# Performance work log

Hardware: AMD Instinct MI355X
Metric: run time of the kernel (lower is better)

Reference implementation:

```python
import jax, jax.numpy as jnp
import numpy as np

# dims: NL layers, D=d_model, DI=expand*D, F=d_ff, V=vocab, L=S*C seq, R=dt_rank, N=d_state, K=d_conv
NL, D, DI, F, V, L, R, N, K = 2, 256, 512, 1024, 1024, 1024, 16, 16, 4
B, S, C = 2, 128, 8
EPS = 1e-5


def silu(x):
    return x * jax.nn.sigmoid(x)


def batchnorm(x, g, b):  # x: [B,L,D], normalize over (B,L) per channel (training-mode BatchNorm1d)
    m = x.mean((0, 1))
    v = x.var((0, 1))
    return (x - m) * jax.lax.rsqrt(v + EPS) * g + b


def layernorm(x, g, b):
    m = x.mean(-1, keepdims=True)
    v = x.var(-1, keepdims=True)
    return (x - m) * jax.lax.rsqrt(v + EPS) * g + b


def mamba(x, Win, cw, cb, Wx, Wdt, bdt, A_log, Dsk, Wout, bout):
    # x: [B,L,D] -> [B,L,D]; standard Mamba block with selective scan
    Bsz, Lseq, _ = x.shape
    xz = x @ Win                      # [B,L,2*DI]
    xi, z = jnp.split(xz, 2, axis=-1)
    # depthwise causal conv1d, width K
    xp = jnp.pad(xi, ((0, 0), (K - 1, 0), (0, 0)))
    xc = cb + sum(xp[:, k:k + Lseq, :] * cw[:, k] for k in range(K))
    xc = silu(xc)                     # [B,L,DI]
    xdb = xc @ Wx                     # [B,L,R+2N]
    delta = jax.nn.softplus(xdb[..., :R] @ Wdt + bdt)   # [B,L,DI]
    Bm = xdb[..., R:R + N]            # [B,L,N]
    Cm = xdb[..., R + N:]             # [B,L,N]
    A = -jnp.exp(A_log)               # [DI,N]
    dA = jnp.exp(delta[..., None] * A)                       # [B,L,DI,N]
    dBx = delta[..., None] * Bm[:, :, None, :] * xc[..., None]  # [B,L,DI,N]

    def step(h, inp):
        dA_t, dBx_t, C_t = inp
        h = h * dA_t + dBx_t          # [B,DI,N]
        y = jnp.einsum('bdn,bn->bd', h, C_t)
        return h, y

    h0 = jnp.zeros((Bsz, DI, N), x.dtype)
    _, ys = jax.lax.scan(step, h0, (dA.transpose(1, 0, 2, 3), dBx.transpose(1, 0, 2, 3), Cm.transpose(1, 0, 2)))
    y = ys.transpose(1, 0, 2) + Dsk * xc
    y = y * silu(z)
    return y @ Wout + bout


def _forward(input_ids, emb, pos, Win, conv_w, conv_b, Wx, Wdt, bdt, A_log, Dskip, Wout, bout,
             bn_g, bn_b, ln_g, ln_b, ff_w1, ff_b1, ff_w2, ff_b2, final_w, final_b):
    Bsz, Ssz, Csz = input_ids.shape
    Lseq = Ssz * Csz
    # Encoder: token embedding (scaled) + learned positions, flattened to [B, S*C, D]
    x = emb[input_ids].reshape(Bsz, Lseq, D) * jnp.sqrt(jnp.float32(D)) + pos[:Lseq]
    for i in range(NL):
        f = mamba(x, Win[i, 0], conv_w[i, 0], conv_b[i, 0], Wx[i, 0], Wdt[i, 0], bdt[i, 0],
                  A_log[i, 0], Dskip[i, 0], Wout[i, 0], bout[i, 0])
        f = batchnorm(f, bn_g[i, 0], bn_b[i, 0])
        bk = mamba(x[:, ::-1], Win[i, 1], conv_w[i, 1], conv_b[i, 1], Wx[i, 1], Wdt[i, 1], bdt[i, 1],
                   A_log[i, 1], Dskip[i, 1], Wout[i, 1], bout[i, 1])
        bk = batchnorm(bk, bn_g[i, 1], bn_b[i, 1])[:, ::-1]
        f = layernorm(x + f, ln_g[i, 0], ln_b[i, 0])
        bk = layernorm(x + bk, ln_g[i, 1], ln_b[i, 1])
        out = f + bk
        out = jax.nn.relu(out @ ff_w1[i] + ff_b1[i]) @ ff_w2[i] + ff_b2[i]
        out = batchnorm(out, bn_g[i, 2], bn_b[i, 2])
        x = out + x
    return x.reshape(Bsz, Ssz, Csz, D) @ final_w + final_b   # [B,S,C,V]


def setup_inputs() -> dict:
    key = jax.random.key(0)
    ks = list(jax.random.split(key, 16))
    kit = iter(ks)
    rn = lambda shape, s=0.02: jax.random.normal(next(kit), shape, jnp.float32) * s
    inp = {
        'input_ids': jax.random.randint(next(kit), (B, S, C), 0, V),
        'emb': rn((V, D)), 'pos': rn((L, D)),
        'Win': rn((NL, 2, D, 2 * DI)),
        'conv_w': rn((NL, 2, DI, K), 0.1), 'conv_b': jnp.zeros((NL, 2, DI)),
        'Wx': rn((NL, 2, DI, R + 2 * N)),
        'Wdt': rn((NL, 2, R, DI)), 'bdt': jnp.full((NL, 2, DI), -4.0),
        'A_log': jnp.broadcast_to(jnp.log(jnp.arange(1, N + 1, dtype=jnp.float32)), (NL, 2, DI, N)) + 0.0,
        'Dskip': jnp.ones((NL, 2, DI)),
        'Wout': rn((NL, 2, DI, D)), 'bout': jnp.zeros((NL, 2, D)),
        'bn_g': jnp.ones((NL, 3, D)), 'bn_b': jnp.zeros((NL, 3, D)),
        'ln_g': jnp.ones((NL, 2, D)), 'ln_b': jnp.zeros((NL, 2, D)),
        'ff_w1': rn((NL, D, F)), 'ff_b1': jnp.zeros((NL, F)),
        'ff_w2': rn((NL, F, D)), 'ff_b2': jnp.zeros((NL, D)),
        'final_w': rn((D, V)), 'final_b': jnp.zeros((V,)),
    }
    return inp


def reference(input_ids, emb, pos, Win, conv_w, conv_b, Wx, Wdt, bdt, A_log, Dskip, Wout, bout,
              bn_g, bn_b, ln_g, ln_b, ff_w1, ff_b1, ff_w2, ff_b2, final_w, final_b):
    return _forward(input_ids, emb, pos, Win, conv_w, conv_b, Wx, Wdt, bdt, A_log, Dskip, Wout, bout,
                    bn_g, bn_b, ln_g, ln_b, ff_w1, ff_b1, ff_w2, ff_b2, final_w, final_b)
```

## Files before the change

kernel.cpp:

```cpp
#include <hip/hip_runtime.h>

#define NL 2
#define DMODEL 256
#define DI 512
#define FF 1024
#define VV 1024
#define LSEQ 1024
#define RR 16
#define NN 16
#define KCONV 4
#define BTOK 2048
#define EPS 1e-5f

using short8 = __attribute__((ext_vector_type(8))) short;
using float4v = __attribute__((ext_vector_type(4))) float;
typedef unsigned short u16;

__device__ inline float bf2f(u16 u) {
    union { unsigned u; float f; } x; x.u = (unsigned)u << 16; return x.f;
}
__device__ inline u16 f2bf(float f) {
    union { float f; unsigned u; } x; x.f = f;
    unsigned r = x.u + 0x7fffu + ((x.u >> 16) & 1u);
    return (u16)(r >> 16);
}

#if __has_builtin(__builtin_amdgcn_exp2f)
#define EXP2(x) __builtin_amdgcn_exp2f(x)
#else
#define EXP2(x) exp2f(x)
#endif

struct TMat { const float* src; u16* dst; int rows, cols, tile0, tilecols; };
struct TTable { TMat m[24]; int nmat; };

__global__ __launch_bounds__(256) void transpose_kernel(TTable tt) {
    __shared__ u16 tile[32][33];
    int bx = blockIdx.x;
    int j = 0;
    for (int k = 1; k < tt.nmat; ++k) if (bx >= tt.m[k].tile0) j = k;
    TMat mm = tt.m[j];
    int lt = bx - mm.tile0;
    int r0 = (lt / mm.tilecols) * 32, c0 = (lt % mm.tilecols) * 32;
    int tx = threadIdx.x & 31, ty = threadIdx.x >> 5;
    #pragma unroll
    for (int k = 0; k < 4; ++k) {
        int r = r0 + ty + k * 8, c = c0 + tx;
        tile[ty + k * 8][tx] = (r < mm.rows && c < mm.cols) ? f2bf(mm.src[(size_t)r * mm.cols + c]) : (u16)0;
    }
    __syncthreads();
    #pragma unroll
    for (int k = 0; k < 4; ++k) {
        int c = c0 + ty + k * 8, r = r0 + tx;
        if (c < mm.cols && r < mm.rows) mm.dst[(size_t)c * mm.rows + r] = tile[tx][ty + k * 8];
    }
}

__global__ __launch_bounds__(256) void gemm_kernel(
    const u16* __restrict__ A0, int lda, unsigned long long sA,
    const u16* __restrict__ B0, int ldb, unsigned long long sB,
    const float* __restrict__ bias0, unsigned long long sBias,
    void* __restrict__ C0, int ldc, unsigned long long sC,
    int M, int N, int K, int act, int outfp)
{
    const u16* A = A0 + (size_t)blockIdx.z * sA;
    const u16* Bt = B0 + (size_t)blockIdx.z * sB;
    const float* bias = bias0 ? (bias0 + (size_t)blockIdx.z * sBias) : nullptr;

    int tid = threadIdx.x;
    int wv = tid >> 6, lane = tid & 63;
    int row0 = blockIdx.y * 64 + (wv >> 1) * 32;
    int col0 = blockIdx.x * 64 + (wv & 1) * 32;
    int mi = lane & 15, kq = lane >> 4;

    float4v acc[2][2];
    #pragma unroll
    for (int a = 0; a < 2; ++a)
        #pragma unroll
        for (int b = 0; b < 2; ++b) acc[a][b] = (float4v){0.f, 0.f, 0.f, 0.f};
    const short8 zer = {0, 0, 0, 0, 0, 0, 0, 0};

    for (int kk = 0; kk < K; kk += 32) {
        int k = kk + kq * 8;
        bool kv = (k < K);
        short8 af[2], bf[2];
        #pragma unroll
        for (int rt = 0; rt < 2; ++rt) {
            int r = row0 + rt * 16 + mi;
            af[rt] = kv ? *(const short8*)(A + (size_t)r * lda + k) : zer;
        }
        #pragma unroll
        for (int ct = 0; ct < 2; ++ct) {
            int n = col0 + ct * 16 + mi;
            bf[ct] = (kv && n < N) ? *(const short8*)(Bt + (size_t)n * ldb + k) : zer;
        }
        #pragma unroll
        for (int rt = 0; rt < 2; ++rt)
            #pragma unroll
            for (int ct = 0; ct < 2; ++ct)
                acc[rt][ct] = __builtin_amdgcn_mfma_f32_16x16x32_bf16(af[rt], bf[ct], acc[rt][ct], 0, 0, 0);
    }

    #pragma unroll
    for (int rt = 0; rt < 2; ++rt)
        #pragma unroll
        for (int ct = 0; ct < 2; ++ct) {
            int n = col0 + ct * 16 + mi;
            if (n >= N) continue;
            float bv = bias ? bias[n] : 0.f;
            #pragma unroll
            for (int r = 0; r < 4; ++r) {
                int m = row0 + rt * 16 + kq * 4 + r;
                float v = acc[rt][ct][r] + bv;
                if (act == 1) v = fmaxf(v, 0.f);
                if (outfp)
                    ((float*)C0)[(size_t)blockIdx.z * sC + (size_t)m * ldc + n] = v;
                else
                    ((u16*)C0)[(size_t)blockIdx.z * sC + (size_t)m * ldc + n] = f2bf(v);
            }
        }
}

__global__ __launch_bounds__(256) void delta_fused_kernel(
    const u16* __restrict__ xdb, const u16* __restrict__ wdtT,
    const float* __restrict__ bdt, const u16* __restrict__ xc,
    u16* __restrict__ deltaT, u16* __restrict__ uT, int layer)
{
    int z = blockIdx.z;
    const u16* A = xdb + (size_t)z * BTOK * 48;
    const u16* Bt = wdtT + (size_t)z * 512 * 16;
    const float* bias = bdt + (size_t)z * 512;

    int tid = threadIdx.x;
    int wv = tid >> 6, lane = tid & 63;
    int row0 = blockIdx.y * 64 + (wv >> 1) * 32;
    int col0 = blockIdx.x * 64 + (wv & 1) * 32;
    int mi = lane & 15, kq = lane >> 4;

    float4v acc[2][2];
    #pragma unroll
    for (int a = 0; a < 2; ++a)
        #pragma unroll
        for (int b = 0; b < 2; ++b) acc[a][b] = (float4v){0.f, 0.f, 0.f, 0.f};
    const short8 zer = {0, 0, 0, 0, 0, 0, 0, 0};

    int k = kq * 8;
    bool kv = (k < 16);
    short8 af[2], bf[2];
    #pragma unroll
    for (int rt = 0; rt < 2; ++rt) {
        int r = row0 + rt * 16 + mi;
        af[rt] = kv ? *(const short8*)(A + (size_t)r * 48 + k) : zer;
    }
    #pragma unroll
    for (int ct = 0; ct < 2; ++ct) {
        int n = col0 + ct * 16 + mi;
        bf[ct] = kv ? *(const short8*)(Bt + (size_t)n * 16 + k) : zer;
    }
    #pragma unroll
    for (int rt = 0; rt < 2; ++rt)
        #pragma unroll
        for (int ct = 0; ct < 2; ++ct)
            acc[rt][ct] = __builtin_amdgcn_mfma_f32_16x16x32_bf16(af[rt], bf[ct], acc[rt][ct], 0, 0, 0);

    #pragma unroll
    for (int rt = 0; rt < 2; ++rt)
        #pragma unroll
        for (int ct = 0; ct < 2; ++ct) {
            int n = col0 + ct * 16 + mi;
            float bv = bias[n];
            #pragma unroll
            for (int r = 0; r < 4; ++r) {
                int m = row0 + rt * 16 + kq * 4 + r;
                float v = acc[rt][ct][r] + bv;
                v = (v > 20.f) ? v : logf(1.f + __expf(v));
                float xcv = bf2f(xc[((size_t)z * BTOK + m) * DI + n]);
                int b = m >> 10, t = m & 1023;
                size_t off = ((size_t)((z * 2 + b) * DI + n)) * LSEQ + t;
                deltaT[off] = f2bf(v);
                uT[off] = f2bf(v * xcv);
            }
        }
}

__global__ __launch_bounds__(256) void embed_kernel(
    const int* __restrict__ ids, const float* __restrict__ emb,
    const float* __restrict__ pos, u16* __restrict__ x)
{
    int tok = blockIdx.x, d = threadIdx.x;
    int id = ids[tok];
    float v = emb[(size_t)id * DMODEL + d] * 16.0f + pos[(size_t)(tok & (LSEQ - 1)) * DMODEL + d];
    x[(size_t)tok * DMODEL + d] = f2bf(v);
}

__global__ __launch_bounds__(256) void conv_kernel(
    const u16* __restrict__ xz, const float* __restrict__ conv_w,
    const float* __restrict__ conv_b, u16* __restrict__ xc, int layer)
{
    unsigned g = blockIdx.x * 256u + threadIdx.x;
    int d = g & 511;
    int t = (g >> 9) & 1023;
    int b = (g >> 19) & 1;
    int dir = g >> 20;
    int wbase = ((layer * 2 + dir) * DI + d);
    float acc = conv_b[wbase];
    int colbase = dir * 1024 + d;
    #pragma unroll
    for (int k = 0; k < KCONV; ++k) {
        int ts = dir ? (t + 3 - k) : (t - 3 + k);
        if (ts >= 0 && ts < LSEQ)
            acc += conv_w[wbase * KCONV + k] * bf2f(xz[(size_t)((b << 10) + ts) * 2048 + colbase]);
    }
    float v = acc / (1.f + __expf(-acc));
    xc[(size_t)(((dir * 2 + b) << 10) + t) * DI + d] = f2bf(v);
}

#define SCC 128
#define SCS 8
#define SLDS (2 * SCC * 17)

template<int DIR>
__device__ __forceinline__ void scan_body(
    const u16* __restrict__ deltaT, const u16* __restrict__ uT,
    const u16* __restrict__ xdb, const float* __restrict__ A_log,
    u16* __restrict__ pT, int layer, int slab,
    float* Ps, float* Qs)
{
    int tid = threadIdx.x;
    int c = tid & 127, dloc = tid >> 7;
    int d = blockIdx.x * 2 + dloc;

    float a2[16];
    const float* al = A_log + (size_t)(((layer * 2 + DIR) * DI + d) * NN);
    #pragma unroll
    for (int n = 0; n < 16; ++n) a2[n] = -__expf(al[n]) * 1.44269504f;

    const size_t tb = ((size_t)(slab * DI + d)) * LSEQ;
    const int rowb = slab << 10;
    const int T0 = DIR ? (1016 - 8 * c) : (8 * c);

    short8 dlv = *(const short8*)(deltaT + tb + T0);
    short8 uvv = *(const short8*)(uT + tb + T0);

    float P[16], Q[16];
    #pragma unroll
    for (int n = 0; n < 16; ++n) { P[n] = 1.f; Q[n] = 0.f; }
    #pragma unroll
    for (int j = 0; j < 8; ++j) {
        const int idx = DIR ? 7 - j : j;
        float dl = bf2f((u16)dlv[idx]);
        float uv = bf2f((u16)uvv[idx]);
        const u16* xr = xdb + (size_t)(rowb + T0 + idx) * 48;
        short8 b0 = *(const short8*)(xr + 16);
        short8 b1 = *(const short8*)(xr + 24);
        #pragma unroll
        for (int n = 0; n < 8; ++n) {
            float dA = EXP2(dl * a2[n]);
            Q[n] = Q[n] * dA + uv * bf2f((u16)b0[n]);
            P[n] *= dA;
        }
        #pragma unroll
        for (int n = 0; n < 8; ++n) {
            float dA = EXP2(dl * a2[8 + n]);
            Q[8 + n] = Q[8 + n] * dA + uv * bf2f((u16)b1[n]);
            P[8 + n] *= dA;
        }
    }
    int base = (dloc * 128 + c) * 17;
    #pragma unroll
    for (int n = 0; n < 16; ++n) { Ps[base + n] = P[n]; Qs[base + n] = Q[n]; }
    __syncthreads();

    if (tid < 32) {
        int n = tid & 15, dl2 = tid >> 4;
        float h = 0.f;
        for (int cc = 0; cc < 128; ++cc) {
            int o = (dl2 * 128 + cc) * 17 + n;
            float p_ = Ps[o], q_ = Qs[o];
            Ps[o] = h;
            h = p_ * h + q_;
        }
    }
    __syncthreads();

    float h[16];
    #pragma unroll
    for (int n = 0; n < 16; ++n) h[n] = Ps[base + n];
    short8 pk;
    #pragma unroll
    for (int j = 0; j < 8; ++j) {
        const int idx = DIR ? 7 - j : j;
        float dl = bf2f((u16)dlv[idx]);
        float uv = bf2f((u16)uvv[idx]);
        const u16* xr = xdb + (size_t)(rowb + T0 + idx) * 48;
        short8 b0 = *(const short8*)(xr + 16);
        short8 b1 = *(const short8*)(xr + 24);
        short8 c0 = *(const short8*)(xr + 32);
        short8 c1 = *(const short8*)(xr + 40);
        float pacc[4] = {0.f, 0.f, 0.f, 0.f};
        #pragma unroll
        for (int n = 0; n < 8; ++n) {
            float dA = EXP2(dl * a2[n]);
            h[n] = h[n] * dA + uv * bf2f((u16)b0[n]);
            pacc[n & 3] = fmaf(h[n], bf2f((u16)c0[n]), pacc[n & 3]);
        }
        #pragma unroll
        for (int n = 0; n < 8; ++n) {
            float dA = EXP2(dl * a2[8 + n]);
            h[8 + n] = h[8 + n] * dA + uv * bf2f((u16)b1[n]);
            pacc[n & 3] = fmaf(h[8 + n], bf2f((u16)c1[n]), pacc[n & 3]);
        }
        pk[idx] = (short)f2bf((pacc[0] + pacc[1]) + (pacc[2] + pacc[3]));
    }
    *(short8*)(pT + tb + T0) = pk;
}

__global__ __launch_bounds__(256) void scan_kernel(
    const u16* __restrict__ deltaT, const u16* __restrict__ uT,
    const u16* __restrict__ xdb, const float* __restrict__ A_log,
    u16* __restrict__ pT, int layer)
{
    __shared__ float Ps[SLDS], Qs[SLDS];
    int slab = blockIdx.y;
    if (slab >> 1)
        scan_body<1>(deltaT, uT, xdb, A_log, pT, layer, slab, Ps, Qs);
    else
        scan_body<0>(deltaT, uT, xdb, A_log, pT, layer, slab, Ps, Qs);
}

__global__ __launch_bounds__(256) void gate_kernel(
    const u16* __restrict__ pT, const u16* __restrict__ xc,
    const u16* __restrict__ xz, const float* __restrict__ Dskip,
    u16* __restrict__ y, int layer)
{
    __shared__ float tile[32][33];
    int z = blockIdx.z, dir = z >> 1, b = z & 1;
    int d0 = blockIdx.x * 32, t0 = blockIdx.y * 32;
    int tx = threadIdx.x & 31, ty = threadIdx.x >> 5;
    #pragma unroll
    for (int k = 0; k < 4; ++k) {
        int d = d0 + ty + k * 8;
        tile[ty + k * 8][tx] = bf2f(pT[((size_t)(z * DI + d)) * LSEQ + t0 + tx]);
    }
    __syncthreads();
    #pragma unroll
    for (int k = 0; k < 4; ++k) {
        int t = t0 + ty + k * 8, d = d0 + tx;
        float p = tile[tx][ty + k * 8];
        float xcv = bf2f(xc[(size_t)((z << 10) + t) * DI + d]);
        float zv = bf2f(xz[(size_t)((b << 10) + t) * 2048 + dir * 1024 + 512 + d]);
        float dsk = Dskip[(layer * 2 + dir) * DI + d];
        float yv = (p + dsk * xcv) * (zv / (1.f + __expf(-zv)));
        y[(size_t)((z << 10) + t) * DI + d] = f2bf(yv);
    }
}

__global__ __launch_bounds__(256) void bnstats_kernel(
    const u16* __restrict__ p0, const u16* __restrict__ p1, float* __restrict__ stats)
{
    int d = blockIdx.x, arr = blockIdx.y, tid = threadIdx.x;
    const u16* p = arr ? p1 : p0;
    float s = 0.f, q = 0.f;
    #pragma unroll
    for (int k = 0; k < 8; ++k) {
        float v = bf2f(p[(size_t)(tid + k * 256) * DMODEL + d]);
        s += v; q += v * v;
    }
    #pragma unroll
    for (int off = 1; off < 64; off <<= 1) { s += __shfl_xor(s, off); q += __shfl_xor(q, off); }
    __shared__ float ss[4], qs[4];
    if ((tid & 63) == 0) { ss[tid >> 6] = s; qs[tid >> 6] = q; }
    __syncthreads();
    if (tid == 0) {
        float S = ss[0] + ss[1] + ss[2] + ss[3];
        float Q2 = qs[0] + qs[1] + qs[2] + qs[3];
        float mean = S * (1.f / 2048.f);
        float var = Q2 * (1.f / 2048.f) - mean * mean;
        stats[(arr * DMODEL + d) * 2] = mean;
        stats[(arr * DMODEL + d) * 2 + 1] = rsqrtf(var + EPS);
    }
}

__global__ __launch_bounds__(256) void fuseln_kernel(
    const u16* __restrict__ x, const u16* __restrict__ outm, const float* __restrict__ stats,
    const float* __restrict__ bng, const float* __restrict__ bnb,
    const float* __restrict__ lng, const float* __restrict__ lnb, u16* __restrict__ ffin)
{
    int tok = blockIdx.x, d = threadIdx.x;
    float xv = bf2f(x[(size_t)tok * DMODEL + d]);
    float of = bf2f(outm[(size_t)tok * DMODEL + d]);
    float ob = bf2f(outm[(size_t)BTOK * DMODEL + (size_t)tok * DMODEL + d]);
    float vf = xv + (of - stats[d * 2]) * stats[d * 2 + 1] * bng[d] + bnb[d];
    float vb = xv + (ob - stats[(DMODEL + d) * 2]) * stats[(DMODEL + d) * 2 + 1] * bng[DMODEL + d] + bnb[DMODEL + d];
    float s0 = vf, s1 = vf * vf, s2 = vb, s3 = vb * vb;
    #pragma unroll
    for (int off = 1; off < 64; off <<= 1) {
        s0 += __shfl_xor(s0, off); s1 += __shfl_xor(s1, off);
        s2 += __shfl_xor(s2, off); s3 += __shfl_xor(s3, off);
    }
    __shared__ float sm[4][4];
    if ((d & 63) == 0) { sm[d >> 6][0] = s0; sm[d >> 6][1] = s1; sm[d >> 6][2] = s2; sm[d >> 6][3] = s3; }
    __syncthreads();
    s0 = sm[0][0] + sm[1][0] + sm[2][0] + sm[3][0];
    s1 = sm[0][1] + sm[1][1] + sm[2][1] + sm[3][1];
    s2 = sm[0][2] + sm[1][2] + sm[2][2] + sm[3][2];
    s3 = sm[0][3] + sm[1][3] + sm[2][3] + sm[3][3];
    float mf = s0 * (1.f / 256.f), vvf = s1 * (1.f / 256.f) - mf * mf;
    float mb = s2 * (1.f / 256.f), vvb = s3 * (1.f / 256.f) - mb * mb;
    float fl = (vf - mf) * rsqrtf(vvf + EPS) * lng[d] + lnb[d];
    float bl = (vb - mb) * rsqrtf(vvb + EPS) * lng[DMODEL + d] + lnb[DMODEL + d];
    ffin[(size_t)tok * DMODEL + d] = f2bf(fl + bl);
}

__global__ __launch_bounds__(256) void bnadd_kernel(
    u16* __restrict__ x, const u16* __restrict__ ffo, const float* __restrict__ stats,
    const float* __restrict__ g, const float* __restrict__ b)
{
    int tok = blockIdx.x, d = threadIdx.x;
    size_t idx = (size_t)tok * DMODEL + d;
    float v = bf2f(x[idx]) + (bf2f(ffo[idx]) - stats[d * 2]) * stats[d * 2 + 1] * g[d] + b[d];
    x[idx] = f2bf(v);
}

extern "C" void kernel_launch(void* const* d_in, const int* in_sizes, int n_in,
                              void* d_out, int out_size, void* d_ws, size_t ws_size,
                              hipStream_t stream)
{
    const int*   ids     = (const int*)d_in[0];
    const float* emb     = (const float*)d_in[1];
    const float* pos     = (const float*)d_in[2];
    const float* Win     = (const float*)d_in[3];
    const float* conv_w  = (const float*)d_in[4];
    const float* conv_b  = (const float*)d_in[5];
    const float* Wx      = (const float*)d_in[6];
    const float* Wdt     = (const float*)d_in[7];
    const float* bdt     = (const float*)d_in[8];
    const float* A_log   = (const float*)d_in[9];
    const float* Dskip   = (const float*)d_in[10];
    const float* Wout    = (const float*)d_in[11];
    const float* bout    = (const float*)d_in[12];
    const float* bn_g    = (const float*)d_in[13];
    const float* bn_b    = (const float*)d_in[14];
    const float* ln_g    = (const float*)d_in[15];
    const float* ln_b    = (const float*)d_in[16];
    const float* ff_w1   = (const float*)d_in[17];
    const float* ff_b1   = (const float*)d_in[18];
    const float* ff_w2   = (const float*)d_in[19];
    const float* ff_b2   = (const float*)d_in[20];
    const float* final_w = (const float*)d_in[21];
    const float* final_b = (const float*)d_in[22];

    char* cur = (char*)d_ws;
    auto alloc = [&](size_t elems) {
        u16* p = (u16*)cur;
        cur += ((elems * 2 + 511) / 512) * 512;
        return p;
    };
    u16* winT  = alloc((size_t)NL * 2048 * 256);
    u16* wxT   = alloc((size_t)NL * 2 * 48 * 512);
    u16* wdtT  = alloc((size_t)NL * 2 * 512 * 16);
    u16* woutT = alloc((size_t)NL * 2 * 256 * 512);
    u16* fw1T  = alloc((size_t)NL * 1024 * 256);
    u16* fw2T  = alloc((size_t)NL * 256 * 1024);
    u16* finT  = alloc((size_t)1024 * 256);
    u16* xbuf   = alloc((size_t)BTOK * DMODEL);
    u16* xz     = alloc((size_t)BTOK * 2048);
    u16* xc     = alloc((size_t)2 * BTOK * DI);
    u16* xdb    = alloc((size_t)2 * BTOK * 48);
    u16* deltaT = alloc((size_t)2 * BTOK * DI);
    u16* uT     = alloc((size_t)2 * BTOK * DI);
    u16* pT     = alloc((size_t)2 * BTOK * DI);
    u16* ybuf   = alloc((size_t)2 * BTOK * DI);
    u16* outm   = alloc((size_t)2 * BTOK * DMODEL);
    u16* ffin   = alloc((size_t)BTOK * DMODEL);
    u16* ffh    = alloc((size_t)BTOK * FF);
    u16* ffo    = alloc((size_t)BTOK * DMODEL);
    float* statsM = (float*)alloc(4096);
    float* statsF = statsM + 1024;

    TTable tt; int nm = 0, tiles = 0;
    auto addT = [&](const float* src, u16* dst, int rows, int cols) {
        int tc = (cols + 31) / 32, tr = (rows + 31) / 32;
        tt.m[nm] = {src, dst, rows, cols, tiles, tc};
        tiles += tc * tr; nm++;
    };
    for (int i = 0; i < NL; ++i) {
        for (int dir = 0; dir < 2; ++dir) {
            addT(Win  + (size_t)(i * 2 + dir) * 256 * 1024, winT  + (size_t)i * 2048 * 256 + (size_t)dir * 1024 * 256, 256, 1024);
            addT(Wx   + (size_t)(i * 2 + dir) * 512 * 48,   wxT   + (size_t)(i * 2 + dir) * 48 * 512,   512, 48);
            addT(Wdt  + (size_t)(i * 2 + dir) * 16 * 512,   wdtT  + (size_t)(i * 2 + dir) * 512 * 16,   16, 512);
            addT(Wout + (size_t)(i * 2 + dir) * 512 * 256,  woutT + (size_t)(i * 2 + dir) * 256 * 512,  512, 256);
        }
        addT(ff_w1 + (size_t)i * 256 * 1024, fw1T + (size_t)i * 1024 * 256, 256, 1024);
        addT(ff_w2 + (size_t)i * 1024 * 256, fw2T + (size_t)i * 256 * 1024, 1024, 256);
    }
    addT(final_w, finT, 256, 1024);
    tt.nmat = nm;
    transpose_kernel<<<tiles, 256, 0, stream>>>(tt);

    embed_kernel<<<BTOK, 256, 0, stream>>>(ids, emb, pos, xbuf);

    auto gemm = [&](const u16* A, int lda, size_t sA, const u16* Bt, int ldb, size_t sB,
                    const float* bias, size_t sBias, void* C, int ldc, size_t sC,
                    int M, int N, int K, int act, int nb, int outfp) {
        dim3 g((N + 63) / 64, M / 64, nb);
        gemm_kernel<<<g, 256, 0, stream>>>(A, lda, (unsigned long long)sA, Bt, ldb, (unsigned long long)sB,
                                           bias, (unsigned long long)sBias, C, ldc, (unsigned long long)sC,
                                           M, N, K, act, outfp);
    };

    for (int i = 0; i < NL; ++i) {
        gemm(xbuf, 256, 0, winT + (size_t)i * 2048 * 256, 256, 0, nullptr, 0,
             xz, 2048, 0, BTOK, 2048, 256, 0, 1, 0);
        conv_kernel<<<(2 * BTOK * DI) / 256, 256, 0, stream>>>(xz, conv_w, conv_b, xc, i);
        gemm(xc, 512, (size_t)BTOK * 512, wxT + (size_t)i * 2 * 48 * 512, 512, 48 * 512,
             nullptr, 0, xdb, 48, (size_t)BTOK * 48, BTOK, 48, 512, 0, 2, 0);
        delta_fused_kernel<<<dim3(8, 32, 2), 256, 0, stream>>>(
            xdb, wdtT + (size_t)i * 2 * 512 * 16, bdt + (size_t)i * 2 * 512, xc, deltaT, uT, i);
        scan_kernel<<<dim3(256, 4), 256, 0, stream>>>(deltaT, uT, xdb, A_log, pT, i);
        gate_kernel<<<dim3(DI / 32, LSEQ / 32, 4), 256, 0, stream>>>(pT, xc, xz, Dskip, ybuf, i);
        gemm(ybuf, 512, (size_t)BTOK * 512, woutT + (size_t)i * 2 * 256 * 512, 512, 256 * 512,
             bout + (size_t)i * 2 * 256, 256, outm, 256, (size_t)BTOK * 256, BTOK, 256, 512, 0, 2, 0);
        bnstats_kernel<<<dim3(256, 2), 256, 0, stream>>>(outm, outm + (size_t)BTOK * 256, statsM);
        fuseln_kernel<<<BTOK, 256, 0, stream>>>(xbuf, outm, statsM,
            bn_g + (size_t)i * 3 * 256, bn_b + (size_t)i * 3 * 256,
            ln_g + (size_t)i * 2 * 256, ln_b + (size_t)i * 2 * 256, ffin);
        gemm(ffin, 256, 0, fw1T + (size_t)i * 1024 * 256, 256, 0,
             ff_b1 + (size_t)i * 1024, 0, ffh, 1024, 0, BTOK, 1024, 256, 1, 1, 0);
        gemm(ffh, 1024, 0, fw2T + (size_t)i * 256 * 1024, 1024, 0,
             ff_b2 + (size_t)i * 256, 0, ffo, 256, 0, BTOK, 256, 1024, 0, 1, 0);
        bnstats_kernel<<<dim3(256, 1), 256, 0, stream>>>(ffo, ffo, statsF);
        bnadd_kernel<<<BTOK, 256, 0, stream>>>(xbuf, ffo, statsF,
            bn_g + (size_t)(i * 3 + 2) * 256, bn_b + (size_t)(i * 3 + 2) * 256);
    }
    gemm(xbuf, 256, 0, finT, 256, 0, final_b, 0,
         d_out, 1024, 0, BTOK, 1024, 256, 0, 1, 1);
}
```

Baseline: 436.6 us.

## Replace serial chunk-carry scan with parallel Hillis-Steele scan in LDS

The cross-chunk carry propagation in the selective scan used to run serially: 32 threads each walked 128 chunks. It is now a log-step Hillis-Steele inclusive scan over all 128 chunk threads, with each block handling one channel (128 threads, 512 blocks). This removes the 128-step serial dependency chain while most threads sat idle. In exchange it adds 14 block barriers, more total LDS traffic and more FMA work per step, and halves the threads per block.

```diff
diff --git a/kernel.cpp b/kernel.cpp
--- a/kernel.cpp
+++ b/kernel.cpp
@@ -215,10 +215,6 @@
     xc[(size_t)(((dir * 2 + b) << 10) + t) * DI + d] = f2bf(v);
 }
 
-#define SCC 128
-#define SCS 8
-#define SLDS (2 * SCC * 17)
-
 template<int DIR>
 __device__ __forceinline__ void scan_body(
     const u16* __restrict__ deltaT, const u16* __restrict__ uT,
@@ -226,9 +222,8 @@
     u16* __restrict__ pT, int layer, int slab,
     float* Ps, float* Qs)
 {
-    int tid = threadIdx.x;
-    int c = tid & 127, dloc = tid >> 7;
-    int d = blockIdx.x * 2 + dloc;
+    int c = threadIdx.x;
+    int d = blockIdx.x;
 
     float a2[16];
     const float* al = A_log + (size_t)(((layer * 2 + DIR) * DI + d) * NN);
@@ -266,26 +261,42 @@
             P[8 + n] *= dA;
         }
     }
-    int base = (dloc * 128 + c) * 17;
+    const int base = c * 17;
     #pragma unroll
     for (int n = 0; n < 16; ++n) { Ps[base + n] = P[n]; Qs[base + n] = Q[n]; }
     __syncthreads();
 
-    if (tid < 32) {
-        int n = tid & 15, dl2 = tid >> 4;
-        float h = 0.f;
-        for (int cc = 0; cc < 128; ++cc) {
-            int o = (dl2 * 128 + cc) * 17 + n;
-            float p_ = Ps[o], q_ = Qs[o];
-            Ps[o] = h;
-            h = p_ * h + q_;
-        }
-    }
-    __syncthreads();
+    for (int off = 1; off < 128; off <<= 1) {
+        float pp[16], qp[16];
+        const bool act = (c >= off);
+        if (act) {
+            int nb = (c - off) * 17;
+            #pragma unroll
+            for (int n = 0; n < 16; ++n) { pp[n] = Ps[nb + n]; qp[n] = Qs[nb + n]; }
+        }
+        __syncthreads();
+        if (act) {
+            #pragma unroll
+            for (int n = 0; n < 16; ++n) {
+                Q[n] = fmaf(P[n], qp[n], Q[n]);
+                P[n] *= pp[n];
+                Ps[base + n] = P[n];
+                Qs[base + n] = Q[n];
+            }
+        }
+        __syncthreads();
+    }
 
     float h[16];
-    #pragma unroll
-    for (int n = 0; n < 16; ++n) h[n] = Ps[base + n];
+    if (c == 0) {
+        #pragma unroll
+        for (int n = 0; n < 16; ++n) h[n] = 0.f;
+    } else {
+        int nb = (c - 1) * 17;
+        #pragma unroll
+        for (int n = 0; n < 16; ++n) h[n] = Qs[nb + n];
+    }
+
     short8 pk;
     #pragma unroll
     for (int j = 0; j < 8; ++j) {
@@ -315,12 +326,12 @@
     *(short8*)(pT + tb + T0) = pk;
 }
 
-__global__ __launch_bounds__(256) void scan_kernel(
+__global__ __launch_bounds__(128) void scan_kernel(
     const u16* __restrict__ deltaT, const u16* __restrict__ uT,
     const u16* __restrict__ xdb, const float* __restrict__ A_log,
     u16* __restrict__ pT, int layer)
 {
-    __shared__ float Ps[SLDS], Qs[SLDS];
+    __shared__ float Ps[128 * 17], Qs[128 * 17];
     int slab = blockIdx.y;
     if (slab >> 1)
         scan_body<1>(deltaT, uT, xdb, A_log, pT, layer, slab, Ps, Qs);
@@ -517,7 +528,7 @@
              nullptr, 0, xdb, 48, (size_t)BTOK * 48, BTOK, 48, 512, 0, 2, 0);
         delta_fused_kernel<<<dim3(8, 32, 2), 256, 0, stream>>>(
             xdb, wdtT + (size_t)i * 2 * 512 * 16, bdt + (size_t)i * 2 * 512, xc, deltaT, uT, i);
-        scan_kernel<<<dim3(256, 4), 256, 0, stream>>>(deltaT, uT, xdb, A_log, pT, i);
+        scan_kernel<<<dim3(512, 4), 128, 0, stream>>>(deltaT, uT, xdb, A_log, pT, i);
         gate_kernel<<<dim3(DI / 32, LSEQ / 32, 4), 256, 0, stream>>>(pT, xc, xz, Dskip, ybuf, i);
         gemm(ybuf, 512, (size_t)BTOK * 512, woutT + (size_t)i * 2 * 256 * 512, 512, 256 * 512,
              bout + (size_t)i * 2 * 256, 256, outm, 256, (size_t)BTOK * 256, BTOK, 256, 512, 0, 2, 0);
```

Result: no change. 444.9 us (+1.9%).
